# Kernel tuning notes

Hardware: AMD Instinct MI355X
Metric: run time of the kernel (lower is better)

## Reference

```python
import jax, jax.numpy as jnp
import numpy as np

N_HEADS = 16

def setup_inputs() -> dict:
    key = jax.random.key(0)
    ks = jax.random.split(key, 9)
    B, L, D = 4, 2048, 1024
    s = D ** -0.5
    return {
        "x": jax.random.normal(ks[0], (B, L, D), dtype=jnp.float32),
        "Wq": jax.random.normal(ks[1], (D, D), dtype=jnp.float32) * s,
        "bq": jax.random.normal(ks[2], (D,), dtype=jnp.float32) * 0.02,
        "Wk": jax.random.normal(ks[3], (D, D), dtype=jnp.float32) * s,
        "bk": jax.random.normal(ks[4], (D,), dtype=jnp.float32) * 0.02,
        "Wv": jax.random.normal(ks[5], (D, D), dtype=jnp.float32) * s,
        "bv": jax.random.normal(ks[6], (D,), dtype=jnp.float32) * 0.02,
        "Wo": jax.random.normal(ks[7], (D, D), dtype=jnp.float32) * s,
        "bo": jax.random.normal(ks[8], (D,), dtype=jnp.float32) * 0.02,
    }

def reference(x, Wq, bq, Wk, bk, Wv, bv, Wo, bo):
    B, L, D = x.shape
    H = N_HEADS
    hd = D // H
    scale = hd ** -0.5
    # torch Linear: y = x @ W.T + b
    q = (x @ Wq.T + bq).reshape(B, L, H, hd)
    k = (x @ Wk.T + bk).reshape(B, L, H, hd)
    v = (x @ Wv.T + bv).reshape(B, L, H, hd)
    # scores [B,H,L,L]
    qk = jnp.einsum('bqhd,bkhd->bhqk', q, k) * scale
    causal = jnp.tril(jnp.ones((L, L), dtype=bool))
    qk = jnp.where(causal[None, None, :, :], qk, -jnp.inf)
    attn = jax.nn.softmax(qk, axis=-1)
    out = jnp.einsum('bhqk,bkhd->bqhd', attn, v).reshape(B, L, D)
    return out @ Wo.T + bo
```

## Files before the change

kernel.cpp:

```cpp
#include <hip/hip_runtime.h>
#include <hip/hip_bf16.h>
#include <math.h>

#define Bsz 4
#define Lsz 2048
#define Dsz 1024
#define Hn 16
#define HDsz 64
#define NQT 16

typedef __attribute__((ext_vector_type(8))) short short8;
typedef __attribute__((ext_vector_type(4))) float floatx4;
typedef __attribute__((ext_vector_type(2))) unsigned uint2v;
typedef unsigned short ushort_t;

__device__ __forceinline__ void load_lds_16B(const void* g, void* l) {
    __builtin_amdgcn_global_load_lds(
        (const __attribute__((address_space(1))) unsigned int*)g,
        (__attribute__((address_space(3))) unsigned int*)l, 16, 0, 0);
}

__device__ inline void cvt_store(float* p, size_t i, float v) { p[i] = v; }
__device__ inline void cvt_store(__hip_bfloat16* p, size_t i, float v) {
    p[i] = __float2bfloat16(v);
}

__device__ inline ushort_t f2bf_raw(float f) {
    __hip_bfloat16 b = __float2bfloat16(f);
    return *reinterpret_cast<ushort_t*>(&b);
}

__device__ inline float bf2f_raw(ushort_t u) {
    union { unsigned int i; float f; } c;
    c.i = ((unsigned int)u) << 16;
    return c.f;
}

__device__ __forceinline__ float fast_exp2(float x) {
#if __has_builtin(__builtin_amdgcn_exp2f)
    return __builtin_amdgcn_exp2f(x);
#else
    return exp2f(x);
#endif
}

__global__ __launch_bounds__(256) void f2ball(
    const float* __restrict__ x, const float* __restrict__ w0,
    const float* __restrict__ w1, const float* __restrict__ w2,
    const float* __restrict__ w3, __hip_bfloat16* __restrict__ xb,
    __hip_bfloat16* __restrict__ wb) {
    int bid = blockIdx.x;
    const float* in;
    __hip_bfloat16* o;
    size_t off;
    if (bid < 8192) {
        off = (size_t)bid * 1024 + threadIdx.x * 4;
        in = x;
        o = xb + off;
    } else {
        int b2 = bid - 8192;
        int sel = b2 >> 10;
        in = sel == 0 ? w0 : (sel == 1 ? w1 : (sel == 2 ? w2 : w3));
        off = (size_t)(b2 & 1023) * 1024 + threadIdx.x * 4;
        o = wb + (size_t)sel * (1024 * 1024) + off;
    }
    float4 v = *(const float4*)(in + off);
    o[0] = __float2bfloat16(v.x);
    o[1] = __float2bfloat16(v.y);
    o[2] = __float2bfloat16(v.z);
    o[3] = __float2bfloat16(v.w);
}

template <typename TO, bool QKV>
__global__ __launch_bounds__(512, 2) void gemm_bt_256(
    const ushort_t* __restrict__ A, const ushort_t* __restrict__ W,
    const float* __restrict__ b0, const float* __restrict__ b1,
    const float* __restrict__ b2, TO* __restrict__ C, int M, int N, int K) {
    __shared__ ushort_t As[2][256 * 64];
    __shared__ ushort_t Bs[2][128 * 64];

    const int t = threadIdx.x;
    const int wave = t >> 6, lane = t & 63;
    const int lmod = lane & 15, quad = lane >> 4;
    const int wm = wave >> 2, wn = wave & 3;

    const int nbn = N >> 7;
    const int nwg = nbn * (M >> 8);
    const int bid = blockIdx.x;
    const int wg = (bid & 7) * (nwg >> 3) + (bid >> 3);
    const int n0 = (wg % nbn) * 128, m0 = (wg / nbn) * 256;

    floatx4 acc[2][2][4] = {};
    short8 Af[4][2], Bf[2];

    const int NT = K >> 6;

    auto stageA = [&](int kt, int bi) {
        const int kk = kt << 6;
#pragma unroll
        for (int p = 0; p < 4; p++) {
            int slot = t + p * 512;
            int row = slot >> 3, c8 = slot & 7;
            int gc8 = c8 ^ (row & 7);
            load_lds_16B(A + (size_t)(m0 + row) * K + kk + gc8 * 8,
                         &As[bi][slot * 8]);
        }
    };
    auto stageB = [&](int kt, int bi) {
        const int kk = kt << 6;
#pragma unroll
        for (int p = 0; p < 2; p++) {
            int slot = t + p * 512;
            int row = slot >> 3, c8 = slot & 7;
            int gc8 = c8 ^ (row & 7);
            load_lds_16B(W + (size_t)(n0 + row) * K + kk + gc8 * 8,
                         &Bs[bi][slot * 8]);
        }
    };
    auto rdA = [&](int bi, int mh) {
#pragma unroll
        for (int mr = 0; mr < 4; mr++) {
            int row = wm * 128 + mh * 64 + mr * 16 + lmod;
#pragma unroll
            for (int ks = 0; ks < 2; ks++) {
                int sc8 = (ks * 4 + quad) ^ (row & 7);
                Af[mr][ks] = *(const short8*)&As[bi][row * 64 + sc8 * 8];
            }
        }
    };
    auto rdB = [&](int bi, int nh) {
        int row = wn * 32 + nh * 16 + lmod;
#pragma unroll
        for (int ks = 0; ks < 2; ks++) {
            int sc8 = (ks * 4 + quad) ^ (row & 7);
            Bf[ks] = *(const short8*)&Bs[bi][row * 64 + sc8 * 8];
        }
    };
    auto domm = [&](int mh, int nh) {
        __builtin_amdgcn_s_setprio(1);
#pragma unroll
        for (int mr = 0; mr < 4; mr++)
#pragma unroll
            for (int ks = 0; ks < 2; ks++)
                acc[mh][nh][mr] = __builtin_amdgcn_mfma_f32_16x16x32_bf16(
                    Af[mr][ks], Bf[ks], acc[mh][nh][mr], 0, 0, 0);
        __builtin_amdgcn_s_setprio(0);
    };

    stageA(0, 0);
    stageB(0, 0);
    asm volatile("s_waitcnt vmcnt(0)" ::: "memory");
    __builtin_amdgcn_s_barrier();
    asm volatile("" ::: "memory");

#pragma unroll 1
    for (int T = 0; T < NT; T++) {
        const int cur = T & 1, nxt = cur ^ 1;
        const bool pf = (T + 1 < NT);
        rdA(cur, 0);
        rdB(cur, 0);
        if (pf) stageA(T + 1, nxt);
        __builtin_amdgcn_s_barrier();
        __builtin_amdgcn_sched_barrier(0);
        domm(0, 0);
        __builtin_amdgcn_s_barrier();
        rdB(cur, 1);
        if (pf) stageB(T + 1, nxt);
        __builtin_amdgcn_s_barrier();
        __builtin_amdgcn_sched_barrier(0);
        domm(0, 1);
        __builtin_amdgcn_s_barrier();
        rdA(cur, 1);
        __builtin_amdgcn_s_barrier();
        __builtin_amdgcn_sched_barrier(0);
        domm(1, 1);
        __builtin_amdgcn_s_barrier();
        rdB(cur, 0);
        __builtin_amdgcn_s_barrier();
        __builtin_amdgcn_sched_barrier(0);
        domm(1, 0);
        asm volatile("s_waitcnt vmcnt(0)" ::: "memory");
        __builtin_amdgcn_s_barrier();
        asm volatile("" ::: "memory");
    }

    const int sec = QKV ? (n0 >> 10) : 0;
    const float* bp = QKV ? (sec == 0 ? b0 : (sec == 1 ? b1 : b2)) : b0;
    TO* Cb = QKV ? (C + (size_t)sec * M * 1024) : C;
    const int Nout = QKV ? 1024 : N;
    const float sc = (QKV && sec == 0) ? 0.1803368801111204f : 1.0f;

#pragma unroll
    for (int mh = 0; mh < 2; mh++)
#pragma unroll
        for (int mr = 0; mr < 4; mr++) {
            int gm = m0 + wm * 128 + mh * 64 + mr * 16 + quad * 4;
#pragma unroll
            for (int nh = 0; nh < 2; nh++) {
                int gn = n0 + wn * 32 + nh * 16 + lmod;
                int cn = QKV ? (gn & 1023) : gn;
                float b = bp[cn];
#pragma unroll
                for (int r = 0; r < 4; r++)
                    cvt_store(Cb, (size_t)(gm + r) * Nout + cn,
                              (acc[mh][nh][mr][r] + b) * sc);
            }
        }
}

__global__ __launch_bounds__(256) void attn_mfma(
    const ushort_t* __restrict__ q, const ushort_t* __restrict__ k,
    const ushort_t* __restrict__ v, ushort_t* __restrict__ Opart,
    float* __restrict__ lpart) {
    __shared__ ushort_t Ks[2][64 * 64];
    __shared__ ushort_t Vs[64 * 64];
    __shared__ ushort_t Ps[4][32 * 64];

    const int t = threadIdx.x;
    const int wave = t >> 6, lane = t & 63;
    const int lmod = lane & 15, quad = lane >> 4;

    const int bid = blockIdx.x;
    const int j = bid >> 3;
    const int bx = j & 15;
    const int p = bx & 7, s = bx >> 3;
    const int bh = (bid & 7) + ((j >> 4) << 3);
    const int b = bh >> 4, h = bh & 15;
    const size_t base = ((size_t)b * Lsz) * Dsz + h * HDsz;

    ushort_t* Pw = (ushort_t*)Ps[wave];
    const int lm7 = lmod & 7;

    auto stageK = [&](int kt, int bi) {
#pragma unroll
        for (int pp = 0; pp < 2; pp++) {
            int slot = t + pp * 256;
            int row = slot >> 3, c8 = slot & 7;
            int gc8 = c8 ^ (row & 7);
            load_lds_16B(k + base + (size_t)(kt * 64 + row) * Dsz + gc8 * 8,
                         &Ks[bi][slot * 8]);
        }
    };
    auto stageV = [&](int kt) {
#pragma unroll
        for (int pp = 0; pp < 2; pp++) {
            int slot = t + pp * 256;
            int row = slot >> 3, c8 = slot & 7;
            int gc8 = c8 ^ (row & 7);
            load_lds_16B(v + base + (size_t)(kt * 64 + row) * Dsz + gc8 * 8,
                         &Vs[slot * 8]);
        }
    };

    const unsigned vsbase =
        (unsigned)(size_t)(__attribute__((address_space(3))) const ushort_t*)Vs;
    unsigned vaddr[2][2][4];
    {
        const int lq = lmod >> 2;
        const int lmb = (lmod & 3) >> 1;
        const int lob = (lmod & 1) * 8;
#pragma unroll
        for (int ks = 0; ks < 2; ks++)
#pragma unroll
            for (int jj = 0; jj < 2; jj++) {
                int rowk = ks * 32 + quad * 8 + jj * 4 + lq;
                int r7 = rowk & 7;
#pragma unroll
                for (int on = 0; on < 4; on++)
                    vaddr[ks][jj][on] = vsbase + rowk * 128 +
                                        (((on * 2 + lmb) ^ r7) << 4) + lob;
            }
    }

    int bi = 0;

    stageK(s * (NQT - p), 0);

#pragma unroll 1
    for (int seg = 0; seg < 2; seg++) {
        const int qtile = seg == 0 ? (NQT - 1 - p) : p;
        const int q0 = qtile * 128;
        const int Th = qtile + 1;
        const int kt0 = s * Th, kt1 = kt0 + Th;
        const int kt0n = s * (p + 1);

        short8 aq[2][2];
#pragma unroll
        for (int g = 0; g < 2; g++) {
            const ushort_t* qp = q + base +
                                 (size_t)(q0 + wave * 32 + g * 16 + lmod) * Dsz +
                                 quad * 8;
            aq[g][0] = *(const short8*)(qp);
            aq[g][1] = *(const short8*)(qp + 32);
        }

        floatx4 Oacc[2][4] = {};
        float lsum[2] = {0.f, 0.f};

#pragma unroll 1
        for (int kt = kt0; kt < kt1; kt++) {
            asm volatile("s_waitcnt vmcnt(0)" ::: "memory");
            __builtin_amdgcn_s_barrier();
            asm volatile("" ::: "memory");

            stageV(kt);
            const int ktn = (kt + 1 < kt1) ? kt + 1 : (seg == 0 ? kt0n : -1);
            if (ktn >= 0) stageK(ktn, bi ^ 1);

            floatx4 St[2][4] = {};
#pragma unroll
            for (int nt = 0; nt < 4; nt++) {
                int key = nt * 16 + lmod;
#pragma unroll
                for (int ks = 0; ks < 2; ks++) {
                    int sc8 = (ks * 4 + quad) ^ (key & 7);
                    short8 kf = *(const short8*)&Ks[bi][(key * 8 + sc8) * 8];
#pragma unroll
                    for (int g = 0; g < 2; g++)
                        St[g][nt] = __builtin_amdgcn_mfma_f32_16x16x32_bf16(
                            kf, aq[g][ks], St[g][nt], 0, 0, 0);
                }
            }

            const bool need_mask = (kt >= 2 * qtile);
#pragma unroll
            for (int g = 0; g < 2; g++) {
                int qg = q0 + wave * 32 + g * 16 + lmod;
#pragma unroll
                for (int nt = 0; nt < 4; nt++) {
                    int k0g = kt * 64 + nt * 16 + quad * 4;
                    float p0 = fast_exp2(St[g][nt][0]);
                    float p1 = fast_exp2(St[g][nt][1]);
                    float p2 = fast_exp2(St[g][nt][2]);
                    float p3 = fast_exp2(St[g][nt][3]);
                    if (need_mask) {
                        if (k0g + 0 > qg) p0 = 0.f;
                        if (k0g + 1 > qg) p1 = 0.f;
                        if (k0g + 2 > qg) p2 = 0.f;
                        if (k0g + 3 > qg) p3 = 0.f;
                    }
                    lsum[g] += ((p0 + p1) + (p2 + p3));
                    unsigned wx, wy;
                    asm("v_cvt_pk_bf16_f32 %0, %1, %2"
                        : "=v"(wx)
                        : "v"(p0), "v"(p1));
                    asm("v_cvt_pk_bf16_f32 %0, %1, %2"
                        : "=v"(wy)
                        : "v"(p2), "v"(p3));
                    uint2 w;
                    w.x = wx;
                    w.y = wy;
                    int c8 = nt * 2 + (quad >> 1);
                    int sc8 = c8 ^ lm7;
                    *(uint2*)&Pw[((g * 16 + lmod) * 8 + sc8) * 8 +
                                 (quad & 1) * 4] = w;
                }
            }

            short8 ap[2][2];
#pragma unroll
            for (int g = 0; g < 2; g++)
#pragma unroll
                for (int ks = 0; ks < 2; ks++) {
                    int sc8 = (ks * 4 + quad) ^ lm7;
                    ap[g][ks] =
                        *(const short8*)&Pw[((g * 16 + lmod) * 8 + sc8) * 8];
                }

            if (ktn >= 0)
                asm volatile("s_waitcnt vmcnt(2)" ::: "memory");
            else
                asm volatile("s_waitcnt vmcnt(0)" ::: "memory");
            __builtin_amdgcn_s_barrier();
            asm volatile("" ::: "memory");

#pragma unroll
            for (int on = 0; on < 4; on++) {
                uint2v t00, t01, t10, t11;
                asm volatile("ds_read_b64_tr_b16 %0, %1"
                             : "=v"(t00)
                             : "v"(vaddr[0][0][on]));
                asm volatile("ds_read_b64_tr_b16 %0, %1"
                             : "=v"(t01)
                             : "v"(vaddr[0][1][on]));
                asm volatile("ds_read_b64_tr_b16 %0, %1"
                             : "=v"(t10)
                             : "v"(vaddr[1][0][on]));
                asm volatile("ds_read_b64_tr_b16 %0, %1"
                             : "=v"(t11)
                             : "v"(vaddr[1][1][on]));
                asm volatile("s_waitcnt lgkmcnt(0)" ::: "memory");
                __builtin_amdgcn_sched_barrier(0);
                union U { uint2v pr[2]; short8 s8; } u0, u1;
                u0.pr[0] = t00;
                u0.pr[1] = t01;
                u1.pr[0] = t10;
                u1.pr[1] = t11;
#pragma unroll
                for (int g = 0; g < 2; g++) {
                    Oacc[g][on] = __builtin_amdgcn_mfma_f32_16x16x32_bf16(
                        ap[g][0], u0.s8, Oacc[g][on], 0, 0, 0);
                    Oacc[g][on] = __builtin_amdgcn_mfma_f32_16x16x32_bf16(
                        ap[g][1], u1.s8, Oacc[g][on], 0, 0, 0);
                }
            }

            bi ^= 1;
        }

#pragma unroll
        for (int g = 0; g < 2; g++) {
            lsum[g] += __shfl_xor(lsum[g], 16);
            lsum[g] += __shfl_xor(lsum[g], 32);
        }

        const size_t rec = ((size_t)bh * NQT + qtile) * 2 + s;
        ushort_t* Orec = Opart + rec * (128 * 64);
        float* lrec = lpart + rec * 128;
#pragma unroll
        for (int g = 0; g < 2; g++) {
            if (quad == 0) lrec[wave * 32 + g * 16 + lmod] = lsum[g];
#pragma unroll
            for (int r = 0; r < 4; r++) {
                int row = wave * 32 + g * 16 + quad * 4 + r;
#pragma unroll
                for (int on = 0; on < 4; on++) {
                    int d = on * 16 + lmod;
                    Orec[row * 64 + d] = f2bf_raw(Oacc[g][on][r]);
                }
            }
        }
    }
}

__global__ __launch_bounds__(256) void attn_combine(
    const ushort_t* __restrict__ Opart, const float* __restrict__ lpart,
    ushort_t* __restrict__ ao) {
    int gidx = blockIdx.x * 256 + threadIdx.x;
    int rowglob = gidx >> 3;
    int c8 = (gidx & 7) * 8;
    int bh = rowglob >> 11;
    int r11 = rowglob & 2047;
    int qtile = r11 >> 7, row = r11 & 127;

    size_t rec0 = ((size_t)bh * NQT + qtile) * 2;
    const ushort_t* O0 = Opart + (rec0 + 0) * (128 * 64) + row * 64 + c8;
    const ushort_t* O1 = Opart + (rec0 + 1) * (128 * 64) + row * 64 + c8;
    float l = lpart[(rec0 + 0) * 128 + row] + lpart[(rec0 + 1) * 128 + row];
    float inv = 1.0f / l;

    short8 a = *(const short8*)O0;
    short8 bvec = *(const short8*)O1;
    short8 o;
#pragma unroll
    for (int j = 0; j < 8; j++) {
        float vv = (bf2f_raw((ushort_t)a[j]) + bf2f_raw((ushort_t)bvec[j])) * inv;
        o[j] = (short)f2bf_raw(vv);
    }
    int b = bh >> 4, h = bh & 15;
    int qg = qtile * 128 + row;
    *(short8*)&ao[((size_t)(b * Lsz + qg)) * Dsz + h * HDsz + c8] = o;
}

extern "C" void kernel_launch(void* const* d_in, const int* in_sizes, int n_in,
                              void* d_out, int out_size, void* d_ws,
                              size_t ws_size, hipStream_t stream) {
    const size_t elems = (size_t)Bsz * Lsz * Dsz;
    const size_t welem = (size_t)Dsz * Dsz;
    const size_t nrec = (size_t)Bsz * Hn * NQT * 2;
    const size_t opart_e = nrec * 128 * 64;
    const size_t need = (5 * elems + 4 * welem + opart_e) * 2 + nrec * 128 * 4;
    if (ws_size < need) return;

    const float* x = (const float*)d_in[0];
    const float* Wq = (const float*)d_in[1];
    const float* bq = (const float*)d_in[2];
    const float* Wk = (const float*)d_in[3];
    const float* bk = (const float*)d_in[4];
    const float* Wv = (const float*)d_in[5];
    const float* bv = (const float*)d_in[6];
    const float* Wo = (const float*)d_in[7];
    const float* bo = (const float*)d_in[8];
    float* out = (float*)d_out;

    __hip_bfloat16* xb = (__hip_bfloat16*)d_ws;
    __hip_bfloat16* q = xb + elems;
    __hip_bfloat16* k = q + elems;
    __hip_bfloat16* v = k + elems;
    __hip_bfloat16* ao = v + elems;
    __hip_bfloat16* Wqb = ao + elems;
    __hip_bfloat16* Wkb = Wqb + welem;
    __hip_bfloat16* Wvb = Wkb + welem;
    __hip_bfloat16* Wob = Wvb + welem;
    ushort_t* Opart = (ushort_t*)(Wob + welem);
    float* lpart = (float*)(Opart + opart_e);

    const int M = Bsz * Lsz, N = Dsz, K = Dsz;

    f2ball<<<12288, 256, 0, stream>>>(x, Wq, Wk, Wv, Wo, xb, Wqb);

    gemm_bt_256<__hip_bfloat16, true><<<(3 * N / 128) * (M / 256), 512, 0,
                                        stream>>>(
        (const ushort_t*)xb, (const ushort_t*)Wqb, bq, bk, bv, q, M, 3 * N, K);

    attn_mfma<<<16 * Bsz * Hn, 256, 0, stream>>>(
        (const ushort_t*)q, (const ushort_t*)k, (const ushort_t*)v, Opart,
        lpart);

    attn_combine<<<(int)(elems / 8 / 256), 256, 0, stream>>>(Opart, lpart,
                                                             (ushort_t*)ao);

    gemm_bt_256<float, false><<<(N / 128) * (M / 256), 512, 0, stream>>>(
        (const ushort_t*)ao, (const ushort_t*)Wob, bo, bo, bo, out, M, N, K);
}
```

Before: 279.3 us.

## Fuse split-KV attention combine into output projection GEMM A-tile staging

```diff
diff --git a/kernel.cpp b/kernel.cpp
--- a/kernel.cpp
+++ b/kernel.cpp
@@ -204,6 +204,174 @@
                 for (int r = 0; r < 4; r++)
                     cvt_store(Cb, (size_t)(gm + r) * Nout + cn,
                               (acc[mh][nh][mr][r] + b) * sc);
+            }
+        }
+}
+
+__global__ __launch_bounds__(512, 2) void gemm_out_fused(
+    const ushort_t* __restrict__ Op, const float* __restrict__ lp,
+    const ushort_t* __restrict__ W, const float* __restrict__ bo,
+    float* __restrict__ C, int M, int N, int K) {
+    __shared__ ushort_t As[2][256 * 64];
+    __shared__ ushort_t Bs[2][128 * 64];
+
+    const int t = threadIdx.x;
+    const int wave = t >> 6, lane = t & 63;
+    const int lmod = lane & 15, quad = lane >> 4;
+    const int wm = wave >> 2, wn = wave & 3;
+
+    const int nbn = N >> 7;
+    const int nwg = nbn * (M >> 8);
+    const int bid = blockIdx.x;
+    const int wg = (bid & 7) * (nwg >> 3) + (bid >> 3);
+    const int n0 = (wg % nbn) * 128, m0 = (wg / nbn) * 256;
+
+    floatx4 acc[2][2][4] = {};
+    short8 Af[4][2], Bf[2];
+
+    const int NT = K >> 6;
+
+    uint4 a0s[4], a1s[4];
+    float l0s[4], l1s[4];
+
+    auto stageA_load = [&](int kt) {
+#pragma unroll
+        for (int p = 0; p < 4; p++) {
+            int slot = t + p * 512;
+            int row = slot >> 3, c8 = slot & 7;
+            int gc8 = c8 ^ (row & 7);
+            int gm = m0 + row;
+            int bq = gm >> 11;
+            int qg = gm & 2047;
+            int qtile = qg >> 7, r128 = qg & 127;
+            size_t rec0 = ((size_t)(bq * Hn + kt) * NQT + qtile) * 2;
+            const ushort_t* O0 = Op + rec0 * 8192 + r128 * 64 + gc8 * 8;
+            a0s[p] = *(const uint4*)O0;
+            a1s[p] = *(const uint4*)(O0 + 8192);
+            l0s[p] = lp[rec0 * 128 + r128];
+            l1s[p] = lp[(rec0 + 1) * 128 + r128];
+        }
+    };
+    auto stageA_write = [&](int bi) {
+#pragma unroll
+        for (int p = 0; p < 4; p++) {
+            int slot = t + p * 512;
+            float inv = 1.0f / (l0s[p] + l1s[p]);
+            unsigned u0[4] = {a0s[p].x, a0s[p].y, a0s[p].z, a0s[p].w};
+            unsigned u1[4] = {a1s[p].x, a1s[p].y, a1s[p].z, a1s[p].w};
+            unsigned w[4];
+#pragma unroll
+            for (int jj = 0; jj < 4; jj++) {
+                float lo = (bf2f_raw((ushort_t)(u0[jj] & 0xffffu)) +
+                            bf2f_raw((ushort_t)(u1[jj] & 0xffffu))) *
+                           inv;
+                float hi = (bf2f_raw((ushort_t)(u0[jj] >> 16)) +
+                            bf2f_raw((ushort_t)(u1[jj] >> 16))) *
+                           inv;
+                asm("v_cvt_pk_bf16_f32 %0, %1, %2"
+                    : "=v"(w[jj])
+                    : "v"(lo), "v"(hi));
+            }
+            uint4 wv;
+            wv.x = w[0];
+            wv.y = w[1];
+            wv.z = w[2];
+            wv.w = w[3];
+            *(uint4*)&As[bi][slot * 8] = wv;
+        }
+    };
+    auto stageB = [&](int kt, int bi) {
+        const int kk = kt << 6;
+#pragma unroll
+        for (int p = 0; p < 2; p++) {
+            int slot = t + p * 512;
+            int row = slot >> 3, c8 = slot & 7;
+            int gc8 = c8 ^ (row & 7);
+            load_lds_16B(W + (size_t)(n0 + row) * K + kk + gc8 * 8,
+                         &Bs[bi][slot * 8]);
+        }
+    };
+    auto rdA = [&](int bi, int mh) {
+#pragma unroll
+        for (int mr = 0; mr < 4; mr++) {
+            int row = wm * 128 + mh * 64 + mr * 16 + lmod;
+#pragma unroll
+            for (int ks = 0; ks < 2; ks++) {
+                int sc8 = (ks * 4 + quad) ^ (row & 7);
+                Af[mr][ks] = *(const short8*)&As[bi][row * 64 + sc8 * 8];
+            }
+        }
+    };
+    auto rdB = [&](int bi, int nh) {
+        int row = wn * 32 + nh * 16 + lmod;
+#pragma unroll
+        for (int ks = 0; ks < 2; ks++) {
+            int sc8 = (ks * 4 + quad) ^ (row & 7);
+            Bf[ks] = *(const short8*)&Bs[bi][row * 64 + sc8 * 8];
+        }
+    };
+    auto domm = [&](int mh, int nh) {
+        __builtin_amdgcn_s_setprio(1);
+#pragma unroll
+        for (int mr = 0; mr < 4; mr++)
+#pragma unroll
+            for (int ks = 0; ks < 2; ks++)
+                acc[mh][nh][mr] = __builtin_amdgcn_mfma_f32_16x16x32_bf16(
+                    Af[mr][ks], Bf[ks], acc[mh][nh][mr], 0, 0, 0);
+        __builtin_amdgcn_s_setprio(0);
+    };
+
+    stageA_load(0);
+    stageA_write(0);
+    stageB(0, 0);
+    asm volatile("s_waitcnt vmcnt(0) lgkmcnt(0)" ::: "memory");
+    __builtin_amdgcn_s_barrier();
+    asm volatile("" ::: "memory");
+
+#pragma unroll 1
+    for (int T = 0; T < NT; T++) {
+        const int cur = T & 1, nxt = cur ^ 1;
+        const bool pf = (T + 1 < NT);
+        rdA(cur, 0);
+        rdB(cur, 0);
+        if (pf) stageA_load(T + 1);
+        __builtin_amdgcn_s_barrier();
+        __builtin_amdgcn_sched_barrier(0);
+        domm(0, 0);
+        __builtin_amdgcn_s_barrier();
+        rdB(cur, 1);
+        if (pf) stageB(T + 1, nxt);
+        __builtin_amdgcn_s_barrier();
+        __builtin_amdgcn_sched_barrier(0);
+        domm(0, 1);
+        __builtin_amdgcn_s_barrier();
+        rdA(cur, 1);
+        __builtin_amdgcn_s_barrier();
+        __builtin_amdgcn_sched_barrier(0);
+        domm(1, 1);
+        __builtin_amdgcn_s_barrier();
+        rdB(cur, 0);
+        __builtin_amdgcn_s_barrier();
+        __builtin_amdgcn_sched_barrier(0);
+        domm(1, 0);
+        if (pf) stageA_write(nxt);
+        asm volatile("s_waitcnt vmcnt(0) lgkmcnt(0)" ::: "memory");
+        __builtin_amdgcn_s_barrier();
+        asm volatile("" ::: "memory");
+    }
+
+#pragma unroll
+    for (int mh = 0; mh < 2; mh++)
+#pragma unroll
+        for (int mr = 0; mr < 4; mr++) {
+            int gm = m0 + wm * 128 + mh * 64 + mr * 16 + quad * 4;
+#pragma unroll
+            for (int nh = 0; nh < 2; nh++) {
+                int gn = n0 + wn * 32 + nh * 16 + lmod;
+                float b = bo[gn];
+#pragma unroll
+                for (int r = 0; r < 4; r++)
+                    C[(size_t)(gm + r) * N + gn] = acc[mh][nh][mr][r] + b;
             }
         }
 }
@@ -433,35 +601,6 @@
     }
 }
 
-__global__ __launch_bounds__(256) void attn_combine(
-    const ushort_t* __restrict__ Opart, const float* __restrict__ lpart,
-    ushort_t* __restrict__ ao) {
-    int gidx = blockIdx.x * 256 + threadIdx.x;
-    int rowglob = gidx >> 3;
-    int c8 = (gidx & 7) * 8;
-    int bh = rowglob >> 11;
-    int r11 = rowglob & 2047;
-    int qtile = r11 >> 7, row = r11 & 127;
-
-    size_t rec0 = ((size_t)bh * NQT + qtile) * 2;
-    const ushort_t* O0 = Opart + (rec0 + 0) * (128 * 64) + row * 64 + c8;
-    const ushort_t* O1 = Opart + (rec0 + 1) * (128 * 64) + row * 64 + c8;
-    float l = lpart[(rec0 + 0) * 128 + row] + lpart[(rec0 + 1) * 128 + row];
-    float inv = 1.0f / l;
-
-    short8 a = *(const short8*)O0;
-    short8 bvec = *(const short8*)O1;
-    short8 o;
-#pragma unroll
-    for (int j = 0; j < 8; j++) {
-        float vv = (bf2f_raw((ushort_t)a[j]) + bf2f_raw((ushort_t)bvec[j])) * inv;
-        o[j] = (short)f2bf_raw(vv);
-    }
-    int b = bh >> 4, h = bh & 15;
-    int qg = qtile * 128 + row;
-    *(short8*)&ao[((size_t)(b * Lsz + qg)) * Dsz + h * HDsz + c8] = o;
-}
-
 extern "C" void kernel_launch(void* const* d_in, const int* in_sizes, int n_in,
                               void* d_out, int out_size, void* d_ws,
                               size_t ws_size, hipStream_t stream) {
@@ -507,9 +646,6 @@
         (const ushort_t*)q, (const ushort_t*)k, (const ushort_t*)v, Opart,
         lpart);
 
-    attn_combine<<<(int)(elems / 8 / 256), 256, 0, stream>>>(Opart, lpart,
-                                                             (ushort_t*)ao);
-
-    gemm_bt_256<float, false><<<(N / 128) * (M / 256), 512, 0, stream>>>(
-        (const ushort_t*)ao, (const ushort_t*)Wob, bo, bo, bo, out, M, N, K);
-}
+    gemm_out_fused<<<(N / 128) * (M / 256), 512, 0, stream>>>(
+        Opart, lpart, (const ushort_t*)Wob, bo, out, M, N, K);
+}
```

After: 284.5 us. No clear change (+1.9%).
